# Performance work log

Hardware: AMD Instinct MI355X
Metric: run time of the kernel (lower is better)

## Reference

```python
import jax, jax.numpy as jnp
import numpy as np

B, S, D, H = 1, 4096, 1024, 16
HD = D // H  # head_dim = 64


def setup_inputs() -> dict:
    key = jax.random.key(0)
    k1, k2, k3 = jax.random.split(key, 3)
    scale = 0.02
    return {
        "x": jax.random.normal(k1, (B, S, D), dtype=jnp.float32),
        "w_qkv": jax.random.normal(k2, (D, 3 * D), dtype=jnp.float32) * scale,
        "b_qkv": jnp.zeros((3 * D,), dtype=jnp.float32),
        "w_proj": jax.random.normal(k3, (D, D), dtype=jnp.float32) * scale,
        "b_proj": jnp.zeros((D,), dtype=jnp.float32),
    }


def reference(x, w_qkv, b_qkv, w_proj, b_proj):
    b, s, d = x.shape
    qkv = x @ w_qkv + b_qkv                      # [b, s, 3d]
    q, k, v = jnp.split(qkv, 3, axis=-1)
    # [b, h, s, hd]
    q = q.reshape(b, s, H, HD).transpose(0, 2, 1, 3)
    k = k.reshape(b, s, H, HD).transpose(0, 2, 1, 3)
    v = v.reshape(b, s, H, HD).transpose(0, 2, 1, 3)
    score = jnp.einsum("bhqd,bhkd->bhqk", q, k) / jnp.sqrt(jnp.float32(HD))
    causal = jnp.tril(jnp.ones((s, s), dtype=bool))
    score = jnp.where(causal, score, -jnp.inf)
    attn = jax.nn.softmax(score, axis=-1)        # dropout omitted (eval mode, p effectively 0)
    out = jnp.einsum("bhqk,bhkd->bhqd", attn, v)  # [b, h, s, hd]
    out = out.transpose(0, 2, 1, 3).reshape(b, s, d)
    return out @ w_proj + b_proj
```

## Files before the change

### kernel.cpp

```cpp
#include <hip/hip_runtime.h>
#include <hip/hip_bf16.h>
#include <math.h>

typedef __bf16 bf16;
typedef __bf16 bf16x8 __attribute__((ext_vector_type(8)));
typedef __bf16 bf16x4 __attribute__((ext_vector_type(4)));
typedef float f32x4 __attribute__((ext_vector_type(4)));
typedef unsigned int u32;
typedef u32 u32x4 __attribute__((ext_vector_type(4)));

#define S_ 4096
#define D_ 1024
#define H_ 16
#define HD_ 64
#define N3_ 3072
#define NSPLIT 4

typedef const __attribute__((address_space(1))) void* gas1_t;
typedef __attribute__((address_space(3))) void* las3_t;
static __device__ __forceinline__ void g2l16(const void* g, void* l) {
  __builtin_amdgcn_global_load_lds((gas1_t)g, (las3_t)l, 16, 0, 0);
}

static __device__ __forceinline__ u32 fbits(float x) {
  union { float f; u32 u; } c; c.f = x; return c.u;
}

__global__ __launch_bounds__(256) void prep_kernel(const float* __restrict__ x,
                                                   bf16* __restrict__ xb,
                                                   const float* __restrict__ w_qkv,
                                                   bf16* __restrict__ wqkvT,
                                                   const float* __restrict__ w_proj,
                                                   bf16* __restrict__ wprojT) {
  __shared__ float t[32][33];
  const int b = blockIdx.x;
  if (b < 4096) {
    int i = (b * 256 + threadIdx.x) * 4;
    float4 v = *(const float4*)(x + i);
    bf16x4 o;
    o.x = (bf16)v.x; o.y = (bf16)v.y; o.z = (bf16)v.z; o.w = (bf16)v.w;
    *(bf16x4*)(xb + i) = o;
    return;
  }
  const float* in; bf16* outp; int ldin, bx, by;
  if (b < 7168) { int b2 = b - 4096; in = w_qkv;  outp = wqkvT;  ldin = N3_; bx = (b2 % 96) * 32; by = (b2 / 96) * 32; }
  else          { int b3 = b - 7168; in = w_proj; outp = wprojT; ldin = D_;  bx = (b3 % 32) * 32; by = (b3 / 32) * 32; }
  const int tx = threadIdx.x & 31, ty = threadIdx.x >> 5;
#pragma unroll
  for (int i = 0; i < 4; ++i)
    t[ty + i * 8][tx] = in[(size_t)(by + ty + i * 8) * ldin + bx + tx];
  __syncthreads();
#pragma unroll
  for (int i = 0; i < 4; ++i)
    outp[(size_t)(bx + ty + i * 8) * D_ + by + tx] = (bf16)t[tx][ty + i * 8];
}

template <int BN>
__global__ __launch_bounds__(256) void gemm_bt(const bf16* __restrict__ A,
                                               const bf16* __restrict__ Bt,
                                               const float* __restrict__ bias,
                                               bf16* __restrict__ outb,
                                               float* __restrict__ outf,
                                               bf16* __restrict__ vF,
                                               int M, int N, int K,
                                               int qlim, float qscale) {
  constexpr int NT = BN / 32;
  __shared__ bf16 sA[128 * 32];
  __shared__ bf16 sB[BN * 32];
  const int tid = threadIdx.x;
  const int wave = tid >> 6, lane = tid & 63;
  const int col = lane & 15, quad = lane >> 4;
  const int wm = (wave & 1) * 64, wn = (wave >> 1) * (BN / 2);
  const long bm = (long)blockIdx.x * 128, bn = (long)blockIdx.y * BN;
  const int srow = tid >> 2;
  const int soff = (tid & 3) * 8;

  f32x4 acc[4][NT] = {};

  for (int kb = 0; kb < K; kb += 32) {
    __syncthreads();
    g2l16(A + (bm + srow) * (long)K + kb + soff,      &sA[tid * 8]);
    g2l16(A + (bm + 64 + srow) * (long)K + kb + soff, &sA[2048 + tid * 8]);
#pragma unroll
    for (int i = 0; i < BN / 64; ++i)
      g2l16(Bt + (bn + i * 64 + srow) * (long)K + kb + soff, &sB[i * 2048 + tid * 8]);
    __syncthreads();

    bf16x8 af[4], bfr[NT];
#pragma unroll
    for (int t = 0; t < 4; ++t)
      af[t] = *(const bf16x8*)(&sA[(wm + t * 16 + col) * 32 + quad * 8]);
#pragma unroll
    for (int t = 0; t < NT; ++t)
      bfr[t] = *(const bf16x8*)(&sB[(wn + t * 16 + col) * 32 + quad * 8]);
#pragma unroll
    for (int mt = 0; mt < 4; ++mt)
#pragma unroll
      for (int nt = 0; nt < NT; ++nt)
        acc[mt][nt] = __builtin_amdgcn_mfma_f32_16x16x32_bf16(af[mt], bfr[nt], acc[mt][nt], 0, 0, 0);
  }

#pragma unroll
  for (int mt = 0; mt < 4; ++mt) {
#pragma unroll
    for (int nt = 0; nt < NT; ++nt) {
      long gn = bn + wn + nt * 16 + col;
      float bv = bias ? bias[gn] : 0.f;
      if (vF && gn >= 2 * D_) {
        int hd = (int)gn - 2 * D_;
        int hh2 = hd >> 6, nn = (hd >> 4) & 3, colp = hd & 15;
        long key0 = bm + wm + mt * 16 + quad * 4;
        int kb64 = (int)(key0 >> 6), kl = (int)(key0 & 63);
        int cc = kl >> 5, qp2 = (kl >> 3) & 3, j0 = kl & 7;
        bf16x4 vv;
#pragma unroll
        for (int i = 0; i < 4; ++i) vv[i] = (bf16)(acc[mt][nt][i] + bv);
        *(bf16x4*)(&vF[((((size_t)(hh2 * 64 + kb64) * 2 + cc) * 4 + nn) * 64 +
                        qp2 * 16 + colp) * 8 + j0]) = vv;
      } else {
        float sc = (gn < qlim) ? qscale : 1.0f;
#pragma unroll
        for (int i = 0; i < 4; ++i) {
          long gm = bm + wm + mt * 16 + quad * 4 + i;
          float v = (acc[mt][nt][i] + bv) * sc;
          if (outf) outf[gm * N + gn] = v;
          else      outb[gm * N + gn] = (bf16)v;
        }
      }
    }
  }
}

__global__ __launch_bounds__(256) void repackK(const bf16* __restrict__ qkv,
                                               bf16* __restrict__ kF) {
  __shared__ bf16 sK[64 * 72];
  const int hh = blockIdx.x, kb64 = blockIdx.y;
  const int tid = threadIdx.x;
  const int srow = tid >> 2, sc = (tid & 3) * 16;
  const bf16* src = qkv + (size_t)(kb64 * 64 + srow) * N3_ + D_ + hh * HD_ + sc;
  *(int4*)(&sK[srow * 72 + sc])     = *(const int4*)src;
  *(int4*)(&sK[srow * 72 + sc + 8]) = *(const int4*)(src + 8);
  __syncthreads();
  const int lane = tid & 63, col = lane & 15, quad = lane >> 4;
  const int t = tid >> 6;
  const int row = (t >> 1) * 32 + (t & 1) * 4 + (col >> 2) * 8 + (col & 3);
  bf16* dst = kF + ((size_t)(hh * 64 + kb64) * 8 + t * 2) * 512 + lane * 8;
  *(bf16x8*)(dst)       = *(const bf16x8*)(&sK[row * 72 + quad * 8]);
  *(bf16x8*)(dst + 512) = *(const bf16x8*)(&sK[row * 72 + 32 + quad * 8]);
}

__global__ __launch_bounds__(128) void attn_kernel(const bf16* __restrict__ qkv,
                                                   const bf16* __restrict__ kF,
                                                   const bf16* __restrict__ vF,
                                                   bf16* __restrict__ Opart,
                                                   float* __restrict__ lws) {
  const int hh = blockIdx.x;
  const int qp = (int)(gridDim.y - 1 - blockIdx.y);
  const int sp = blockIdx.z;
  const int tid = threadIdx.x;
  const int wave = tid >> 6, lane = tid & 63;
  const int col = lane & 15, quad = lane >> 4;
  const int qbase = qp * 64 + wave * 32;

  const bf16* qp0 = qkv + (size_t)(qbase + col) * N3_ + hh * HD_;
  bf16x8 aq[2][2];
  aq[0][0] = *(const bf16x8*)(qp0 + quad * 8);
  aq[0][1] = *(const bf16x8*)(qp0 + 32 + quad * 8);
  aq[1][0] = *(const bf16x8*)(qp0 + 16 * N3_ + quad * 8);
  aq[1][1] = *(const bf16x8*)(qp0 + 16 * N3_ + 32 + quad * 8);

  bf16x8 ones;
#pragma unroll
  for (int j = 0; j < 8; ++j) ones[j] = (bf16)1.0f;

  f32x4 acc[2][4] = {};
  f32x4 acc_l[2] = {};

  const int niter = qp + 1;
  const int bse = niter >> 2, rem = niter & 3;
  const int it0 = sp * bse + (sp < rem ? sp : rem);
  const int len = bse + (sp < rem ? 1 : 0);
  const int it1 = it0 + len;

  const bf16* kfp = kF + (size_t)(hh * 64 + it0) * 4096 + lane * 8;
  const bf16* vfp = vF + (size_t)(hh * 64 + it0) * 4096 + lane * 8;

  for (int j = it0; j < it1; ++j, kfp += 4096, vfp += 4096) {
    const int kb = j * 64;
    if (kb >= qbase + 32) break;
    const bool act0 = kb < qbase + 16;

    f32x4 st[2][4];
#pragma unroll
    for (int t = 0; t < 4; ++t) {
      bf16x8 bk0 = *(const bf16x8*)(kfp + (t * 2) * 512);
      bf16x8 bk1 = *(const bf16x8*)(kfp + (t * 2 + 1) * 512);
      if (act0) {
        f32x4 z = {};
        z = __builtin_amdgcn_mfma_f32_16x16x32_bf16(bk0, aq[0][0], z, 0, 0, 0);
        st[0][t] = __builtin_amdgcn_mfma_f32_16x16x32_bf16(bk1, aq[0][1], z, 0, 0, 0);
      }
      f32x4 z = {};
      z = __builtin_amdgcn_mfma_f32_16x16x32_bf16(bk0, aq[1][0], z, 0, 0, 0);
      st[1][t] = __builtin_amdgcn_mfma_f32_16x16x32_bf16(bk1, aq[1][1], z, 0, 0, 0);
    }

    bf16x8 pfrag[2][2];
#pragma unroll
    for (int s2 = 0; s2 < 2; ++s2) {
      if (s2 == 0 && !act0) continue;
      const int rowbase = qbase + 16 * s2;
      float p[4][4];
      if (kb + 63 <= rowbase) {
#pragma unroll
        for (int t = 0; t < 4; ++t)
#pragma unroll
          for (int r = 0; r < 4; ++r)
            p[t][r] = __builtin_amdgcn_exp2f(st[s2][t][r]);
      } else {
#pragma unroll
        for (int t = 0; t < 4; ++t)
#pragma unroll
          for (int r = 0; r < 4; ++r) {
            int key = kb + (t >> 1) * 32 + quad * 8 + (t & 1) * 4 + r;
            p[t][r] = (key > rowbase + col)
                          ? 0.f
                          : __builtin_amdgcn_exp2f(st[s2][t][r]);
          }
      }
#pragma unroll
      for (int c = 0; c < 2; ++c) {
        union { bf16x8 v; u32x4 u; } pu;
        pu.u[0] = __builtin_amdgcn_perm(fbits(p[2 * c][1]),     fbits(p[2 * c][0]),     0x07060302u);
        pu.u[1] = __builtin_amdgcn_perm(fbits(p[2 * c][3]),     fbits(p[2 * c][2]),     0x07060302u);
        pu.u[2] = __builtin_amdgcn_perm(fbits(p[2 * c + 1][1]), fbits(p[2 * c + 1][0]), 0x07060302u);
        pu.u[3] = __builtin_amdgcn_perm(fbits(p[2 * c + 1][3]), fbits(p[2 * c + 1][2]), 0x07060302u);
        pfrag[s2][c] = pu.v;
      }
    }

#pragma unroll
    for (int c = 0; c < 2; ++c) {
#pragma unroll
      for (int n = 0; n < 4; ++n) {
        bf16x8 bv = *(const bf16x8*)(vfp + (c * 4 + n) * 512);
        if (act0)
          acc[0][n] = __builtin_amdgcn_mfma_f32_16x16x32_bf16(pfrag[0][c], bv, acc[0][n], 0, 0, 0);
        acc[1][n] = __builtin_amdgcn_mfma_f32_16x16x32_bf16(pfrag[1][c], bv, acc[1][n], 0, 0, 0);
      }
      if (act0)
        acc_l[0] = __builtin_amdgcn_mfma_f32_16x16x32_bf16(pfrag[0][c], ones, acc_l[0], 0, 0, 0);
      acc_l[1] = __builtin_amdgcn_mfma_f32_16x16x32_bf16(pfrag[1][c], ones, acc_l[1], 0, 0, 0);
    }
  }

  bf16* Op = Opart + (size_t)sp * S_ * D_;
#pragma unroll
  for (int s2 = 0; s2 < 2; ++s2) {
    const int rowbase = qbase + 16 * s2;
    if (col == 0) {
#pragma unroll
      for (int r = 0; r < 4; ++r)
        lws[((size_t)sp * H_ + hh) * S_ + rowbase + quad * 4 + r] = acc_l[s2][r];
    }
#pragma unroll
    for (int n = 0; n < 4; ++n)
#pragma unroll
      for (int r = 0; r < 4; ++r)
        Op[(size_t)(rowbase + quad * 4 + r) * D_ + hh * HD_ + n * 16 + col] =
            (bf16)acc[s2][n][r];
  }
}

__global__ __launch_bounds__(256) void attn_combine(const bf16* __restrict__ Opart,
                                                    const float* __restrict__ lws,
                                                    bf16* __restrict__ outb) {
  int e = (blockIdx.x * 256 + threadIdx.x) * 8;
  int s = e >> 10;
  int h = (e & (D_ - 1)) >> 6;
  float l = 0.f;
#pragma unroll
  for (int sp = 0; sp < NSPLIT; ++sp) l += lws[((size_t)sp * H_ + h) * S_ + s];
  float inv = 1.0f / l;
  float o[8] = {};
#pragma unroll
  for (int sp = 0; sp < NSPLIT; ++sp) {
    bf16x8 a = *(const bf16x8*)(Opart + (size_t)sp * S_ * D_ + e);
#pragma unroll
    for (int j = 0; j < 8; ++j) o[j] += (float)a[j];
  }
  bf16x8 r;
#pragma unroll
  for (int j = 0; j < 8; ++j) r[j] = (bf16)(o[j] * inv);
  *(bf16x8*)(outb + e) = r;
}

extern "C" void kernel_launch(void* const* d_in, const int* in_sizes, int n_in,
                              void* d_out, int out_size, void* d_ws, size_t ws_size,
                              hipStream_t stream) {
  const float* x      = (const float*)d_in[0];
  const float* w_qkv  = (const float*)d_in[1];
  const float* b_qkv  = (const float*)d_in[2];
  const float* w_proj = (const float*)d_in[3];
  const float* b_proj = (const float*)d_in[4];
  float* out = (float*)d_out;

  bf16* xb     = (bf16*)d_ws;
  bf16* wqkvT  = xb + (size_t)S_ * D_;
  bf16* wprojT = wqkvT + (size_t)N3_ * D_;
  bf16* qkv    = wprojT + (size_t)D_ * D_;
  bf16* vF     = qkv + (size_t)S_ * N3_;
  bf16* Opart  = vF + (size_t)D_ * S_;
  float* lws   = (float*)(Opart + (size_t)NSPLIT * S_ * D_);
  bf16* kF     = xb;
  bf16* attn   = xb;

  const float QSCALE = 0.125f * 1.44269504088896f;

  prep_kernel<<<dim3(8192), 256, 0, stream>>>(x, xb, w_qkv, wqkvT, w_proj, wprojT);
  gemm_bt<128><<<dim3(S_ / 128, N3_ / 128), 256, 0, stream>>>(
      xb, wqkvT, b_qkv, qkv, nullptr, vF, S_, N3_, D_, D_, QSCALE);
  repackK<<<dim3(H_, S_ / 64), 256, 0, stream>>>(qkv, kF);
  attn_kernel<<<dim3(H_, S_ / 64, NSPLIT), 128, 0, stream>>>(qkv, kF, vF, Opart, lws);
  attn_combine<<<dim3((S_ * D_) / 2048), 256, 0, stream>>>(Opart, lws, attn);
  gemm_bt<64><<<dim3(S_ / 128, D_ / 64), 256, 0, stream>>>(
      attn, wprojT, b_proj, nullptr, out, nullptr, S_, D_, D_, 0, 1.0f);
}
```

Baseline: 216.7 us.

## Software-pipeline K loads and QK MFMAs one key block ahead in attention loop

Restructures the attention inner loop so the next key block's K fragments are loaded and its QK^T MFMAs issued after the current PV step, overlapping global load latency with compute. The act0 predicate is dropped, so both 16-row subtiles are always computed, and causal masking is applied only on the diagonal block (j == qp). This raises register pressure (bk[8], bv[8] held live) and adds redundant work for the first subtile on the diagonal block.

New measurement: 214.2 us. Within noise of the previous version (-1.2%).

```diff
diff --git a/kernel.cpp b/kernel.cpp
--- a/kernel.cpp
+++ b/kernel.cpp
@@ -182,75 +182,109 @@
   const int len = bse + (sp < rem ? 1 : 0);
   const int it1 = it0 + len;
 
-  const bf16* kfp = kF + (size_t)(hh * 64 + it0) * 4096 + lane * 8;
-  const bf16* vfp = vF + (size_t)(hh * 64 + it0) * 4096 + lane * 8;
-
-  for (int j = it0; j < it1; ++j, kfp += 4096, vfp += 4096) {
-    const int kb = j * 64;
-    if (kb >= qbase + 32) break;
-    const bool act0 = kb < qbase + 16;
+  if (len > 0) {
+    const bf16* kfp = kF + (size_t)(hh * 64 + it0) * 4096 + lane * 8;
+    const bf16* vfp = vF + (size_t)(hh * 64 + it0) * 4096 + lane * 8;
+
+    bf16x8 bk[8];
+#pragma unroll
+    for (int t = 0; t < 8; ++t) bk[t] = *(const bf16x8*)(kfp + t * 512);
+    kfp += 4096;
 
     f32x4 st[2][4];
 #pragma unroll
     for (int t = 0; t < 4; ++t) {
-      bf16x8 bk0 = *(const bf16x8*)(kfp + (t * 2) * 512);
-      bf16x8 bk1 = *(const bf16x8*)(kfp + (t * 2 + 1) * 512);
-      if (act0) {
-        f32x4 z = {};
-        z = __builtin_amdgcn_mfma_f32_16x16x32_bf16(bk0, aq[0][0], z, 0, 0, 0);
-        st[0][t] = __builtin_amdgcn_mfma_f32_16x16x32_bf16(bk1, aq[0][1], z, 0, 0, 0);
-      }
       f32x4 z = {};
-      z = __builtin_amdgcn_mfma_f32_16x16x32_bf16(bk0, aq[1][0], z, 0, 0, 0);
-      st[1][t] = __builtin_amdgcn_mfma_f32_16x16x32_bf16(bk1, aq[1][1], z, 0, 0, 0);
+      z = __builtin_amdgcn_mfma_f32_16x16x32_bf16(bk[2 * t], aq[0][0], z, 0, 0, 0);
+      st[0][t] = __builtin_amdgcn_mfma_f32_16x16x32_bf16(bk[2 * t + 1], aq[0][1], z, 0, 0, 0);
+      f32x4 z2 = {};
+      z2 = __builtin_amdgcn_mfma_f32_16x16x32_bf16(bk[2 * t], aq[1][0], z2, 0, 0, 0);
+      st[1][t] = __builtin_amdgcn_mfma_f32_16x16x32_bf16(bk[2 * t + 1], aq[1][1], z2, 0, 0, 0);
     }
 
-    bf16x8 pfrag[2][2];
-#pragma unroll
-    for (int s2 = 0; s2 < 2; ++s2) {
-      if (s2 == 0 && !act0) continue;
-      const int rowbase = qbase + 16 * s2;
-      float p[4][4];
-      if (kb + 63 <= rowbase) {
-#pragma unroll
-        for (int t = 0; t < 4; ++t)
-#pragma unroll
-          for (int r = 0; r < 4; ++r)
-            p[t][r] = __builtin_amdgcn_exp2f(st[s2][t][r]);
+    for (int j = it0; j < it1; ++j) {
+      const bool more = (j + 1 < it1);
+      const int kb = j * 64;
+
+      bf16x8 bv[8];
+#pragma unroll
+      for (int t = 0; t < 8; ++t) bv[t] = *(const bf16x8*)(vfp + t * 512);
+      vfp += 4096;
+
+      if (more) {
+#pragma unroll
+        for (int t = 0; t < 8; ++t) bk[t] = *(const bf16x8*)(kfp + t * 512);
+        kfp += 4096;
+      }
+
+      bf16x8 pfrag[2][2];
+      if (j == qp) {
+#pragma unroll
+        for (int s2 = 0; s2 < 2; ++s2) {
+          const int rowbase = qbase + 16 * s2;
+          float p[4][4];
+#pragma unroll
+          for (int t = 0; t < 4; ++t)
+#pragma unroll
+            for (int r = 0; r < 4; ++r) {
+              int key = kb + (t >> 1) * 32 + quad * 8 + (t & 1) * 4 + r;
+              p[t][r] = (key > rowbase + col)
+                            ? 0.f
+                            : __builtin_amdgcn_exp2f(st[s2][t][r]);
+            }
+#pragma unroll
+          for (int c = 0; c < 2; ++c) {
+            union { bf16x8 v; u32x4 u; } pu;
+            pu.u[0] = __builtin_amdgcn_perm(fbits(p[2 * c][1]),     fbits(p[2 * c][0]),     0x07060302u);
+            pu.u[1] = __builtin_amdgcn_perm(fbits(p[2 * c][3]),     fbits(p[2 * c][2]),     0x07060302u);
+            pu.u[2] = __builtin_amdgcn_perm(fbits(p[2 * c + 1][1]), fbits(p[2 * c + 1][0]), 0x07060302u);
+            pu.u[3] = __builtin_amdgcn_perm(fbits(p[2 * c + 1][3]), fbits(p[2 * c + 1][2]), 0x07060302u);
+            pfrag[s2][c] = pu.v;
+          }
+        }
       } else {
 #pragma unroll
-        for (int t = 0; t < 4; ++t)
-#pragma unroll
-          for (int r = 0; r < 4; ++r) {
-            int key = kb + (t >> 1) * 32 + quad * 8 + (t & 1) * 4 + r;
-            p[t][r] = (key > rowbase + col)
-                          ? 0.f
-                          : __builtin_amdgcn_exp2f(st[s2][t][r]);
+        for (int s2 = 0; s2 < 2; ++s2) {
+          float p[4][4];
+#pragma unroll
+          for (int t = 0; t < 4; ++t)
+#pragma unroll
+            for (int r = 0; r < 4; ++r)
+              p[t][r] = __builtin_amdgcn_exp2f(st[s2][t][r]);
+#pragma unroll
+          for (int c = 0; c < 2; ++c) {
+            union { bf16x8 v; u32x4 u; } pu;
+            pu.u[0] = __builtin_amdgcn_perm(fbits(p[2 * c][1]),     fbits(p[2 * c][0]),     0x07060302u);
+            pu.u[1] = __builtin_amdgcn_perm(fbits(p[2 * c][3]),     fbits(p[2 * c][2]),     0x07060302u);
+            pu.u[2] = __builtin_amdgcn_perm(fbits(p[2 * c + 1][1]), fbits(p[2 * c + 1][0]), 0x07060302u);
+            pu.u[3] = __builtin_amdgcn_perm(fbits(p[2 * c + 1][3]), fbits(p[2 * c + 1][2]), 0x07060302u);
+            pfrag[s2][c] = pu.v;
           }
-      }
+        }
+      }
+
 #pragma unroll
       for (int c = 0; c < 2; ++c) {
-        union { bf16x8 v; u32x4 u; } pu;
-        pu.u[0] = __builtin_amdgcn_perm(fbits(p[2 * c][1]),     fbits(p[2 * c][0]),     0x07060302u);
-        pu.u[1] = __builtin_amdgcn_perm(fbits(p[2 * c][3]),     fbits(p[2 * c][2]),     0x07060302u);
-        pu.u[2] = __builtin_amdgcn_perm(fbits(p[2 * c + 1][1]), fbits(p[2 * c + 1][0]), 0x07060302u);
-        pu.u[3] = __builtin_amdgcn_perm(fbits(p[2 * c + 1][3]), fbits(p[2 * c + 1][2]), 0x07060302u);
-        pfrag[s2][c] = pu.v;
-      }
-    }
-
-#pragma unroll
-    for (int c = 0; c < 2; ++c) {
-#pragma unroll
-      for (int n = 0; n < 4; ++n) {
-        bf16x8 bv = *(const bf16x8*)(vfp + (c * 4 + n) * 512);
-        if (act0)
-          acc[0][n] = __builtin_amdgcn_mfma_f32_16x16x32_bf16(pfrag[0][c], bv, acc[0][n], 0, 0, 0);
-        acc[1][n] = __builtin_amdgcn_mfma_f32_16x16x32_bf16(pfrag[1][c], bv, acc[1][n], 0, 0, 0);
-      }
-      if (act0)
+#pragma unroll
+        for (int n = 0; n < 4; ++n) {
+          acc[0][n] = __builtin_amdgcn_mfma_f32_16x16x32_bf16(pfrag[0][c], bv[c * 4 + n], acc[0][n], 0, 0, 0);
+          acc[1][n] = __builtin_amdgcn_mfma_f32_16x16x32_bf16(pfrag[1][c], bv[c * 4 + n], acc[1][n], 0, 0, 0);
+        }
         acc_l[0] = __builtin_amdgcn_mfma_f32_16x16x32_bf16(pfrag[0][c], ones, acc_l[0], 0, 0, 0);
-      acc_l[1] = __builtin_amdgcn_mfma_f32_16x16x32_bf16(pfrag[1][c], ones, acc_l[1], 0, 0, 0);
+        acc_l[1] = __builtin_amdgcn_mfma_f32_16x16x32_bf16(pfrag[1][c], ones, acc_l[1], 0, 0, 0);
+      }
+
+      if (more) {
+#pragma unroll
+        for (int t = 0; t < 4; ++t) {
+          f32x4 z = {};
+          z = __builtin_amdgcn_mfma_f32_16x16x32_bf16(bk[2 * t], aq[0][0], z, 0, 0, 0);
+          st[0][t] = __builtin_amdgcn_mfma_f32_16x16x32_bf16(bk[2 * t + 1], aq[0][1], z, 0, 0, 0);
+          f32x4 z2 = {};
+          z2 = __builtin_amdgcn_mfma_f32_16x16x32_bf16(bk[2 * t], aq[1][0], z2, 0, 0, 0);
+          st[1][t] = __builtin_amdgcn_mfma_f32_16x16x32_bf16(bk[2 * t + 1], aq[1][1], z2, 0, 0, 0);
+        }
+      }
     }
   }
 
```
